# Kernel tuning notes

Measured on AMD Instinct MI355X. Metric: run time of the kernel, lower is better.

## Reference

```python
import jax, jax.numpy as jnp
import numpy as np

N_GENE = 50000
N_PROT = 50000
E = 500000
D = 128          # embedding_dim
C = 32           # out_channels = embedding_dim // attn_heads
F_IN = 256       # in_channels per node type
NUM_MP = 3       # metapaths: [gene-gene, gene-protein, protein-protein]


def _glorot(key, shape):
    lim = float(np.sqrt(6.0 / (shape[0] + shape[1])))
    return jax.random.uniform(key, shape, minval=-lim, maxval=lim, dtype=jnp.float32)


def setup_inputs() -> dict:
    key = jax.random.key(0)
    ks = jax.random.split(key, 24)
    inp = {
        "x_gene": jax.random.normal(ks[0], (N_GENE, F_IN), dtype=jnp.float32),
        "x_protein": jax.random.normal(ks[1], (N_PROT, F_IN), dtype=jnp.float32),
        # node-type projections linear_l / linear_r
        "Wl_gene": _glorot(ks[2], (D, F_IN)), "bl_gene": jnp.zeros((D,), jnp.float32),
        "Wr_gene": _glorot(ks[3], (D, F_IN)), "br_gene": jnp.zeros((D,), jnp.float32),
        "Wl_prot": _glorot(ks[4], (D, F_IN)), "bl_prot": jnp.zeros((D,), jnp.float32),
        "Wr_prot": _glorot(ks[5], (D, F_IN)), "br_prot": jnp.zeros((D,), jnp.float32),
        # per-metapath attention params (stacked over 3 metapaths)
        "alW": jnp.stack([_glorot(ks[6 + i], (C, D)) for i in range(NUM_MP)]),
        "alb": jnp.zeros((NUM_MP, C), jnp.float32),
        "arW": jnp.stack([_glorot(ks[9 + i], (C, D)) for i in range(NUM_MP)]),
        "arb": jnp.zeros((NUM_MP, C), jnp.float32),
        "qw": jnp.stack([_glorot(ks[12 + i], (2 * C, 1)) for i in range(NUM_MP)]),
        "sharp": jnp.ones((NUM_MP,), jnp.float32),  # 'sharpening' alpha_activation
        # per-node-type relation-weighting conv (Linear(D, 1))
        "conv_gene_W": _glorot(ks[15], (1, D)), "conv_gene_b": jnp.zeros((1,), jnp.float32),
        "conv_prot_W": _glorot(ks[16], (1, D)), "conv_prot_b": jnp.zeros((1,), jnp.float32),
        # edge indices: row 0 = head node (aggregation target), row 1 = tail node
        "edge_gg": jax.random.randint(ks[17], (2, E), 0, N_GENE, dtype=jnp.int32),
        "edge_gp": jnp.stack([jax.random.randint(ks[18], (E,), 0, N_GENE, dtype=jnp.int32),
                               jax.random.randint(ks[19], (E,), 0, N_PROT, dtype=jnp.int32)]),
        "edge_pp": jax.random.randint(ks[20], (2, E), 0, N_PROT, dtype=jnp.int32),
    }
    return inp


def _segment_softmax(scores, seg, n):
    # numerically stable softmax over variable-size neighborhoods (grouped by seg)
    m = jax.ops.segment_max(scores, seg, num_segments=n)
    m = jnp.where(jnp.isfinite(m), m, 0.0)
    ex = jnp.exp(scores - m[seg])
    denom = jax.ops.segment_sum(ex, seg, num_segments=n)
    return ex / (denom[seg] + 1e-16)


def _metapath_agg(l_head, r_tail, alW, alb, arW, arb, qw, sharp, eidx, n_head):
    # alpha_l / alpha_r node-level projections [N, C]
    al = l_head @ alW.T + alb
    ar = r_tail @ arW.T + arb
    src, dst = eidx[0], eidx[1]           # head (aggregate-at), tail (message-from)
    a_i = al[src]                          # [E, C]
    a_j = ar[dst]                          # [E, C]
    # attn_q: Tanh then Linear(2C -> 1, no bias); 'sharpening' scales the logit
    e = (jnp.tanh(jnp.concatenate([a_i, a_j], axis=1)) @ qw)[:, 0] * sharp  # [E]
    alpha = _segment_softmax(e, src, n_head)
    # message x_j * alpha, scatter-add into head nodes (aggr='add')
    return jax.ops.segment_sum(r_tail[dst] * alpha[:, None], src, num_segments=n_head)


def _relation_combine(aggs, l_self, conv_W, conv_b):
    # stack relation embeddings + self embedding: [N, R, D]
    out = jnp.stack(aggs + [l_self], axis=1)
    beta = jax.nn.softmax(out @ conv_W.T + conv_b, axis=1)  # [N, R, 1]
    return jax.nn.relu(jnp.sum(out * beta, axis=1))          # [N, D]


def reference(x_gene, x_protein, Wl_gene, bl_gene, Wr_gene, br_gene,
              Wl_prot, bl_prot, Wr_prot, br_prot,
              alW, alb, arW, arb, qw, sharp,
              conv_gene_W, conv_gene_b, conv_prot_W, conv_prot_b,
              edge_gg, edge_gp, edge_pp):
    # first layer: l/r projections from raw features
    l_gene = x_gene @ Wl_gene.T + bl_gene
    r_gene = x_gene @ Wr_gene.T + br_gene
    l_prot = x_protein @ Wl_prot.T + bl_prot
    r_prot = x_protein @ Wr_prot.T + br_prot

    # metapath 0: gene <- gene ; metapath 1: gene <- protein ; metapath 2: protein <- protein
    agg_gg = _metapath_agg(l_gene, r_gene, alW[0], alb[0], arW[0], arb[0], qw[0], sharp[0], edge_gg, N_GENE)
    agg_gp = _metapath_agg(l_gene, r_prot, alW[1], alb[1], arW[1], arb[1], qw[1], sharp[1], edge_gp, N_GENE)
    agg_pp = _metapath_agg(l_prot, r_prot, alW[2], alb[2], arW[2], arb[2], qw[2], sharp[2], edge_pp, N_PROT)

    out_gene = _relation_combine([agg_gg, agg_gp], l_gene, conv_gene_W, conv_gene_b)
    out_prot = _relation_combine([agg_pp], l_prot, conv_prot_W, conv_prot_b)
    return (out_gene, out_prot)
```

## Files before the change

kernel.cpp:

```cpp
#include <hip/hip_runtime.h>
#include <hip/hip_bf16.h>


typedef __attribute__((ext_vector_type(8))) short short8;
typedef __attribute__((ext_vector_type(4))) float floatx4;

__device__ __forceinline__ void gload16(const void* g, void* l) {
  __builtin_amdgcn_global_load_lds(
      (const __attribute__((address_space(1))) void*)g,
      (__attribute__((address_space(3))) void*)l, 16, 0, 0);
}

__device__ __forceinline__ ushort f2b(float x) {
  __hip_bfloat16 h = __float2bfloat16(x);
  return *reinterpret_cast<ushort*>(&h);
}
__device__ __forceinline__ float b2f_lo(unsigned v) { return __uint_as_float(v << 16); }
__device__ __forceinline__ float b2f_hi(unsigned v) { return __uint_as_float(v & 0xffff0000u); }

struct CvtArgs {
  const float* src[8];
  ushort* dst[8];
  int valid[8];
  int total[8];
  int bstart[9];
};
__global__ __launch_bounds__(256) void cvt_multi(CvtArgs a) {
  int b = blockIdx.x;
  int e = 0;
#pragma unroll
  for (int j = 1; j < 8; ++j)
    if (b >= a.bstart[j]) e = j;
  int i = ((b - a.bstart[e]) * 256 + threadIdx.x) * 4;
  if (i >= a.total[e]) return;
  float4 v = make_float4(0.f, 0.f, 0.f, 0.f);
  if (i < a.valid[e]) v = *(const float4*)(a.src[e] + i);
  ushort4 o;
  o.x = f2b(v.x); o.y = f2b(v.y); o.z = f2b(v.z); o.w = f2b(v.w);
  *(ushort4*)(a.dst[e] + i) = o;
}

struct ProjArgs {
  const float* x[2];
  const ushort* Wb[2];
  const float* bl[2];
  const float* br[2];
  ushort* lb[2];
  ushort* rb[2];
  int N[2];
  const ushort* aW[4];
  const float* ab[4];
  const float* q0[4];
  const float* q1[4];
  float* o0[4];
  float* o1[4];
  int BN[4];
  const float* sharp;
  const int* e0;
  const int* e1;
  const int* e2;
  int* deg;
  int* rank;
  int E;
  int NGh;
  int projBlocks;
  int totalBlocks;
};
__global__ __launch_bounds__(256) void proj_lr_mfma(ProjArgs g) {
  __shared__ float Asf[2 * 128 * 32];
  __shared__ ushort Bs[2 * 128 * 32];
  const int tid = threadIdx.x;

  const int P = g.projBlocks, T = g.totalBlocks;
  const int bid = blockIdx.x;
  const int pcntLo = (int)(((long long)bid * P) / T);
  const int pcntHi = (int)(((long long)(bid + 1) * P) / T);
  const bool isProj = pcntHi > pcntLo;

  if (!isProj) {
    const int E = g.E;
    int e = (bid - pcntLo) * 256 + tid;
    if (e < 3 * E) {
      int mp = (e >= 2 * E) ? 2 : ((e >= E) ? 1 : 0);
      int el = e - mp * E;
      const int* ep = (mp == 0) ? g.e0 : (mp == 1) ? g.e1 : g.e2;
      int segb = (mp == 2) ? 2 * g.NGh : mp * g.NGh;
      g.rank[e] = atomicAdd(&g.deg[segb + ep[el]], 1);
    }
    return;
  }

  const int pb = pcntLo;
  const int ty = pb & 1;
  const int colHalf = (pb >> 1) & 1;
  const float* xp = g.x[ty];
  const int N = g.N[ty];
  const int lane = tid & 63;
  const int wv = tid >> 6;
  const int wm = wv & 1, wn = wv >> 1;
  const int rowBase = (pb >> 2) * 128;
  const ushort* Wbase = g.Wb[ty] + (size_t)colHalf * 128 * 256;

  floatx4 acc[4][4] = {};

  auto stage = [&](int buf, int k0) {
#pragma unroll
    for (int i = 0; i < 4; ++i) {
      const int G = i * 256 + wv * 64 + lane;
      const int row = G >> 3;
      const int cg = (G & 7) ^ (row & 7);
      const int xr = min(rowBase + row, N - 1);
      gload16(xp + (size_t)xr * 256 + k0 + cg * 4, &Asf[buf * 4096 + G * 4]);
    }
#pragma unroll
    for (int i = 0; i < 2; ++i) {
      const int G = i * 256 + wv * 64 + lane;
      const int row = G >> 2;
      const int cg = (G & 3) ^ ((row >> 1) & 3);
      gload16(Wbase + (size_t)row * 256 + k0 + cg * 8, &Bs[buf * 4096 + G * 8]);
    }
  };

  stage(0, 0);
  __syncthreads();

  int t = 0;
  for (int k0 = 0; k0 < 256; k0 += 32) {
    if (k0 < 224) stage(t ^ 1, k0 + 32);
    const float* Ab = &Asf[t * 4096];
    const ushort* Bb = &Bs[t * 4096];
    short8 bf[4];
#pragma unroll
    for (int nt = 0; nt < 4; ++nt) {
      const int row = wn * 64 + nt * 16 + (lane & 15);
      const int c = (lane >> 4) ^ ((row >> 1) & 3);
      bf[nt] = *(const short8*)&Bb[(row * 4 + c) * 8];
    }
#pragma unroll
    for (int mt = 0; mt < 4; ++mt) {
      const int row = wm * 64 + mt * 16 + (lane & 15);
      const int c0 = ((lane >> 4) * 2) ^ (row & 7);
      const int c1 = ((lane >> 4) * 2 + 1) ^ (row & 7);
      float4 f0 = *(const float4*)&Ab[(row * 8 + c0) * 4];
      float4 f1 = *(const float4*)&Ab[(row * 8 + c1) * 4];
      short8 a;
      a[0] = (short)f2b(f0.x); a[1] = (short)f2b(f0.y);
      a[2] = (short)f2b(f0.z); a[3] = (short)f2b(f0.w);
      a[4] = (short)f2b(f1.x); a[5] = (short)f2b(f1.y);
      a[6] = (short)f2b(f1.z); a[7] = (short)f2b(f1.w);
#pragma unroll
      for (int nt = 0; nt < 4; ++nt)
        acc[mt][nt] = __builtin_amdgcn_mfma_f32_16x16x32_bf16(a, bf[nt], acc[mt][nt], 0, 0, 0);
    }
    __syncthreads();
    t ^= 1;
  }

  ushort* tile = (ushort*)Asf;
  const float* bias = colHalf ? g.br[ty] : g.bl[ty];
  ushort* outp = colHalf ? g.rb[ty] : g.lb[ty];
#pragma unroll
  for (int mt = 0; mt < 4; ++mt)
#pragma unroll
    for (int nt = 0; nt < 4; ++nt) {
      int col = wn * 64 + nt * 16 + (lane & 15);
      float bv = bias[col];
#pragma unroll
      for (int vi = 0; vi < 4; ++vi) {
        int row = wm * 64 + mt * 16 + (lane >> 4) * 4 + vi;
        ushort v = f2b(acc[mt][nt][vi] + bv);
        if (colHalf)
          tile[row * 128 + (((col >> 3) ^ (row & 15)) << 3) + (col & 7)] = v;
        if (rowBase + row < N) outp[(size_t)(rowBase + row) * 128 + col] = v;
      }
    }
  if (colHalf == 0) return;
  __syncthreads();

  const int e = ty * 2 + colHalf;
  const int NB = g.BN[e] >> 4;
  const ushort* aW = g.aW[e];
  floatx4 acc2[2][4] = {};
  for (int k0 = 0; k0 < 128; k0 += 32) {
    short8 bf2[4];
#pragma unroll
    for (int nt = 0; nt < 4; ++nt)
      if (nt < NB)
        bf2[nt] = *(const short8*)(aW + (size_t)(nt * 16 + (lane & 15)) * 128 +
                                   k0 + (lane >> 4) * 8);
#pragma unroll
    for (int mt = 0; mt < 2; ++mt) {
      const int row = wv * 32 + mt * 16 + (lane & 15);
      const int c8 = (k0 >> 3) + (lane >> 4);
      short8 a = *(const short8*)&tile[row * 128 + ((c8 ^ (row & 15)) << 3)];
#pragma unroll
      for (int nt = 0; nt < 4; ++nt)
        if (nt < NB)
          acc2[mt][nt] = __builtin_amdgcn_mfma_f32_16x16x32_bf16(a, bf2[nt], acc2[mt][nt], 0, 0, 0);
    }
  }

  const float* ab = g.ab[e];
  const int l15 = lane & 15;
  const bool two = (NB == 4);
  const float shLo = (e == 1) ? g.sharp[0] : g.sharp[1];
  const float shHi = g.sharp[2];
  float bv2[4];
#pragma unroll
  for (int nt = 0; nt < 4; ++nt) bv2[nt] = (nt < NB) ? ab[nt * 16 + l15] : 0.f;
  float q0v0 = g.q0[e][l15], q0v1 = g.q0[e][16 + l15];
  float q1v0 = 0.f, q1v1 = 0.f;
  if (two) { q1v0 = g.q1[e][l15]; q1v1 = g.q1[e][16 + l15]; }
  float* o0 = g.o0[e];
  float* o1 = g.o1[e];
#pragma unroll
  for (int mt = 0; mt < 2; ++mt)
#pragma unroll
    for (int vi = 0; vi < 4; ++vi) {
      float slo = tanhf(acc2[mt][0][vi] + bv2[0]) * q0v0
                + tanhf(acc2[mt][1][vi] + bv2[1]) * q0v1;
      float shi = 0.f;
      if (two)
        shi = tanhf(acc2[mt][2][vi] + bv2[2]) * q1v0
            + tanhf(acc2[mt][3][vi] + bv2[3]) * q1v1;
#pragma unroll
      for (int m = 8; m >= 1; m >>= 1) {
        slo += __shfl_xor(slo, m, 64);
        shi += __shfl_xor(shi, m, 64);
      }
      const int row = rowBase + wv * 32 + mt * 16 + (lane >> 4) * 4 + vi;
      if (l15 == 0 && row < N) {
        o0[row] = expf(slo * shLo);
        if (two) o1[row] = expf(shi * shHi);
      }
    }
}

__global__ __launch_bounds__(256) void scanA_kernel(
    const int* __restrict__ deg, int* __restrict__ offsets,
    int* __restrict__ tile_tot, int n) {
  __shared__ int wtot[4];
  const int t = threadIdx.x;
  const int base = blockIdx.x * 2048 + t * 8;
  int v[8], pre[8], s = 0;
#pragma unroll
  for (int j = 0; j < 8; ++j) {
    v[j] = (base + j < n) ? deg[base + j] : 0;
    pre[j] = s;
    s += v[j];
  }
  const int lane = t & 63, wv = t >> 6;
  int x = s;
#pragma unroll
  for (int o = 1; o < 64; o <<= 1) {
    int u = __shfl_up(x, o, 64);
    if (lane >= o) x += u;
  }
  if (lane == 63) wtot[wv] = x;
  __syncthreads();
  int wpre = 0;
#pragma unroll
  for (int j = 0; j < 4; ++j) wpre += (j < wv) ? wtot[j] : 0;
  int excl = wpre + x - s;
#pragma unroll
  for (int j = 0; j < 8; ++j)
    if (base + j < n) offsets[base + j] = excl + pre[j];
  if (t == 255) tile_tot[blockIdx.x] = wpre + x;
}

__global__ __launch_bounds__(256) void scanB_kernel(
    const int* __restrict__ tile_tot, int* __restrict__ tile_pre,
    int* __restrict__ offsets, int T, int n) {
  __shared__ int wtot[4];
  const int t = threadIdx.x;
  int v = (t < T) ? tile_tot[t] : 0;
  const int lane = t & 63, wv = t >> 6;
  int x = v;
#pragma unroll
  for (int o = 1; o < 64; o <<= 1) {
    int u = __shfl_up(x, o, 64);
    if (lane >= o) x += u;
  }
  if (lane == 63) wtot[wv] = x;
  __syncthreads();
  int wpre = 0;
#pragma unroll
  for (int j = 0; j < 4; ++j) wpre += (j < wv) ? wtot[j] : 0;
  if (t < T) tile_pre[t] = wpre + x - v;
  if (t == 255) offsets[n] = wpre + x;
}

__global__ __launch_bounds__(256) void scanC_kernel(
    int* __restrict__ offsets, const int* __restrict__ tile_pre, int n) {
  const int add = tile_pre[blockIdx.x];
  const int base = blockIdx.x * 2048 + threadIdx.x * 8;
#pragma unroll
  for (int j = 0; j < 8; ++j)
    if (base + j < n) offsets[base + j] += add;
}

__global__ __launch_bounds__(256) void scatter3_kernel(
    const int* __restrict__ e0, const int* __restrict__ e1,
    const int* __restrict__ e2, const int* __restrict__ rank,
    const int* __restrict__ offsets,
    const float* __restrict__ etr, int2* __restrict__ recs,
    int E, int NG, int NP) {
  int e = blockIdx.x * 256 + threadIdx.x;
  if (e >= 3 * E) return;
  int mp = (e >= 2 * E) ? 2 : ((e >= E) ? 1 : 0);
  int el = e - mp * E;
  const int* ep = (mp == 0) ? e0 : (mp == 1) ? e1 : e2;
  int s = ep[el], d = ep[el + E];
  int hb = (mp == 2) ? 2 * NG : mp * NG;
  int tb = (mp == 0) ? 0 : (mp == 1) ? NG : NG + NP;
  float w = etr[tb + d];
  recs[offsets[hb + s] + rank[e]] = make_int2(d << 8, __float_as_int(w));
}

__global__ __launch_bounds__(256) void gather_combine(
    const ushort* __restrict__ rb_gene, const ushort* __restrict__ rb_prot,
    const ushort* __restrict__ lb_gene, const ushort* __restrict__ lb_prot,
    const int* __restrict__ offsets, const int2* __restrict__ recs,
    const float* __restrict__ cgW, const float* __restrict__ cgb,
    const float* __restrict__ cpW, const float* __restrict__ cpb,
    float* __restrict__ out_gene, float* __restrict__ out_prot,
    int NG, int NP) {
  const int lane = threadIdx.x & 63;
  const int l16 = lane & 15;
  const int node = blockIdx.x * 16 + (threadIdx.x >> 4);
  if (node >= NG + NP) return;
  const bool isGene = node < NG;
  const unsigned coloff = (unsigned)l16 << 4;
  const unsigned OMASK = 0x00FFFF00u;

  const int h0 = isGene ? node : NG + node;
  const int j0a = offsets[h0];
  const int ca = offsets[h0 + 1] - j0a;
  int j0b = 0, cb2 = 0;
  if (isGene) {
    j0b = offsets[NG + node];
    cb2 = offsets[NG + node + 1] - j0b;
  }

  float a0[8] = {0.f, 0.f, 0.f, 0.f, 0.f, 0.f, 0.f, 0.f};
  float a1[8] = {0.f, 0.f, 0.f, 0.f, 0.f, 0.f, 0.f, 0.f};
  float ds0 = 0.f, ds1 = 0.f;
  const ushort* rtA = isGene ? rb_gene : rb_prot;

  if (isGene) {
    const int cmax = (ca > cb2) ? ca : cb2;
    if (cmax > 0) {
      int2 rA[4], rB[4];
#pragma unroll
      for (int p = 0; p < 4; ++p) {
        rA[p] = recs[j0a + ((p < ca) ? p : 0)];
        rB[p] = recs[j0b + ((p < cb2) ? p : 0)];
      }
      const int nit = (cmax + 3) >> 2;
      for (int it = 0; it < nit; ++it) {
        const int b = it * 4;
        float wA[4], wB[4];
        uint4 vA[4], vB[4];
#pragma unroll
        for (int p = 0; p < 4; ++p) {
          wA[p] = (b + p < ca)  ? __int_as_float(rA[p].y) : 0.f;
          wB[p] = (b + p < cb2) ? __int_as_float(rB[p].y) : 0.f;
          vA[p] = *(const uint4*)((const char*)rtA + (((unsigned)rA[p].x & OMASK) + coloff));
          vB[p] = *(const uint4*)((const char*)rb_prot + (((unsigned)rB[p].x & OMASK) + coloff));
        }
        const int nb = b + 4;
#pragma unroll
        for (int p = 0; p < 4; ++p) {
          rA[p] = recs[j0a + ((nb + p < ca) ? nb + p : 0)];
          rB[p] = recs[j0b + ((nb + p < cb2) ? nb + p : 0)];
        }
#pragma unroll
        for (int p = 0; p < 4; ++p) {
          ds0 += wA[p];
          a0[0] += b2f_lo(vA[p].x) * wA[p]; a0[1] += b2f_hi(vA[p].x) * wA[p];
          a0[2] += b2f_lo(vA[p].y) * wA[p]; a0[3] += b2f_hi(vA[p].y) * wA[p];
          a0[4] += b2f_lo(vA[p].z) * wA[p]; a0[5] += b2f_hi(vA[p].z) * wA[p];
          a0[6] += b2f_lo(vA[p].w) * wA[p]; a0[7] += b2f_hi(vA[p].w) * wA[p];
          ds1 += wB[p];
          a1[0] += b2f_lo(vB[p].x) * wB[p]; a1[1] += b2f_hi(vB[p].x) * wB[p];
          a1[2] += b2f_lo(vB[p].y) * wB[p]; a1[3] += b2f_hi(vB[p].y) * wB[p];
          a1[4] += b2f_lo(vB[p].z) * wB[p]; a1[5] += b2f_hi(vB[p].z) * wB[p];
          a1[6] += b2f_lo(vB[p].w) * wB[p]; a1[7] += b2f_hi(vB[p].w) * wB[p];
        }
      }
    }
  } else {
    if (ca > 0) {
      int2 r0 = recs[j0a];
      int2 r1 = recs[j0a + ((1 < ca) ? 1 : 0)];
      int2 r2 = recs[j0a + ((2 < ca) ? 2 : 0)];
      int2 r3 = recs[j0a + ((3 < ca) ? 3 : 0)];
      const int nit = (ca + 3) >> 2;
      for (int it = 0; it < nit; ++it) {
        const int b = it * 4;
        const float w0 = (b < ca)     ? __int_as_float(r0.y) : 0.f;
        const float w1 = (b + 1 < ca) ? __int_as_float(r1.y) : 0.f;
        const float w2 = (b + 2 < ca) ? __int_as_float(r2.y) : 0.f;
        const float w3 = (b + 3 < ca) ? __int_as_float(r3.y) : 0.f;
        const uint4 v0 = *(const uint4*)((const char*)rtA + (((unsigned)r0.x & OMASK) + coloff));
        const uint4 v1 = *(const uint4*)((const char*)rtA + (((unsigned)r1.x & OMASK) + coloff));
        const uint4 v2 = *(const uint4*)((const char*)rtA + (((unsigned)r2.x & OMASK) + coloff));
        const uint4 v3 = *(const uint4*)((const char*)rtA + (((unsigned)r3.x & OMASK) + coloff));
        const int nb = b + 4;
        r0 = recs[j0a + ((nb < ca) ? nb : 0)];
        r1 = recs[j0a + ((nb + 1 < ca) ? nb + 1 : 0)];
        r2 = recs[j0a + ((nb + 2 < ca) ? nb + 2 : 0)];
        r3 = recs[j0a + ((nb + 3 < ca) ? nb + 3 : 0)];
        ds0 += (w0 + w1) + (w2 + w3);
        a0[0] += b2f_lo(v0.x) * w0 + b2f_lo(v1.x) * w1 + b2f_lo(v2.x) * w2 + b2f_lo(v3.x) * w3;
        a0[1] += b2f_hi(v0.x) * w0 + b2f_hi(v1.x) * w1 + b2f_hi(v2.x) * w2 + b2f_hi(v3.x) * w3;
        a0[2] += b2f_lo(v0.y) * w0 + b2f_lo(v1.y) * w1 + b2f_lo(v2.y) * w2 + b2f_lo(v3.y) * w3;
        a0[3] += b2f_hi(v0.y) * w0 + b2f_hi(v1.y) * w1 + b2f_hi(v2.y) * w2 + b2f_hi(v3.y) * w3;
        a0[4] += b2f_lo(v0.z) * w0 + b2f_lo(v1.z) * w1 + b2f_lo(v2.z) * w2 + b2f_lo(v3.z) * w3;
        a0[5] += b2f_hi(v0.z) * w0 + b2f_hi(v1.z) * w1 + b2f_hi(v2.z) * w2 + b2f_hi(v3.z) * w3;
        a0[6] += b2f_lo(v0.w) * w0 + b2f_lo(v1.w) * w1 + b2f_lo(v2.w) * w2 + b2f_lo(v3.w) * w3;
        a0[7] += b2f_hi(v0.w) * w0 + b2f_hi(v1.w) * w1 + b2f_hi(v2.w) * w2 + b2f_hi(v3.w) * w3;
      }
    }
  }

  const float inv0 = 1.f / (ds0 + 1e-16f);
  const float inv1 = 1.f / (ds1 + 1e-16f);
  float g0[8], g1[8], self[8];
#pragma unroll
  for (int c = 0; c < 8; ++c) { g0[c] = a0[c] * inv0; g1[c] = a1[c] * inv1; }
  {
    const ushort* lbp = isGene ? lb_gene + (size_t)node * 128
                               : lb_prot + (size_t)(node - NG) * 128;
    uint4 sv = *(const uint4*)(lbp + l16 * 8);
    self[0] = b2f_lo(sv.x); self[1] = b2f_hi(sv.x);
    self[2] = b2f_lo(sv.y); self[3] = b2f_hi(sv.y);
    self[4] = b2f_lo(sv.z); self[5] = b2f_hi(sv.z);
    self[6] = b2f_lo(sv.w); self[7] = b2f_hi(sv.w);
  }

  const float* cW = isGene ? cgW : cpW;
  const float cb = isGene ? cgb[0] : cpb[0];
  const float4 wlo = *(const float4*)(cW + l16 * 8);
  const float4 whi = *(const float4*)(cW + l16 * 8 + 4);
  float p0 = g0[0] * wlo.x + g0[1] * wlo.y + g0[2] * wlo.z + g0[3] * wlo.w +
             g0[4] * whi.x + g0[5] * whi.y + g0[6] * whi.z + g0[7] * whi.w;
  float p1 = g1[0] * wlo.x + g1[1] * wlo.y + g1[2] * wlo.z + g1[3] * wlo.w +
             g1[4] * whi.x + g1[5] * whi.y + g1[6] * whi.z + g1[7] * whi.w;
  float ps = self[0] * wlo.x + self[1] * wlo.y + self[2] * wlo.z + self[3] * wlo.w +
             self[4] * whi.x + self[5] * whi.y + self[6] * whi.z + self[7] * whi.w;
#pragma unroll
  for (int m = 8; m >= 1; m >>= 1) {
    p0 += __shfl_xor(p0, m, 64);
    p1 += __shfl_xor(p1, m, 64);
    ps += __shfl_xor(ps, m, 64);
  }
  const float s0 = p0 + cb, s1 = p1 + cb, ss = ps + cb;
  const float mx = isGene ? fmaxf(fmaxf(s0, s1), ss) : fmaxf(s0, ss);
  const float e0 = expf(s0 - mx);
  const float e1 = isGene ? expf(s1 - mx) : 0.f;
  const float es = expf(ss - mx);
  const float sum = e0 + e1 + es;
  const float b0 = e0 / sum, b1 = e1 / sum, bs = es / sum;

  float4 o0, o1;
  o0.x = fmaxf(g0[0] * b0 + g1[0] * b1 + self[0] * bs, 0.f);
  o0.y = fmaxf(g0[1] * b0 + g1[1] * b1 + self[1] * bs, 0.f);
  o0.z = fmaxf(g0[2] * b0 + g1[2] * b1 + self[2] * bs, 0.f);
  o0.w = fmaxf(g0[3] * b0 + g1[3] * b1 + self[3] * bs, 0.f);
  o1.x = fmaxf(g0[4] * b0 + g1[4] * b1 + self[4] * bs, 0.f);
  o1.y = fmaxf(g0[5] * b0 + g1[5] * b1 + self[5] * bs, 0.f);
  o1.z = fmaxf(g0[6] * b0 + g1[6] * b1 + self[6] * bs, 0.f);
  o1.w = fmaxf(g0[7] * b0 + g1[7] * b1 + self[7] * bs, 0.f);
  float* op = isGene ? out_gene + (size_t)node * 128
                     : out_prot + (size_t)(node - NG) * 128;
  *(float4*)(op + l16 * 8) = o0;
  *(float4*)(op + l16 * 8 + 4) = o1;
}

extern "C" void kernel_launch(void* const* d_in, const int* in_sizes, int n_in,
                              void* d_out, int out_size, void* d_ws,
                              size_t ws_size, hipStream_t stream) {
  const float* x_gene  = (const float*)d_in[0];
  const float* x_prot  = (const float*)d_in[1];
  const float* Wl_gene = (const float*)d_in[2];
  const float* bl_gene = (const float*)d_in[3];
  const float* Wr_gene = (const float*)d_in[4];
  const float* br_gene = (const float*)d_in[5];
  const float* Wl_prot = (const float*)d_in[6];
  const float* bl_prot = (const float*)d_in[7];
  const float* Wr_prot = (const float*)d_in[8];
  const float* br_prot = (const float*)d_in[9];
  const float* alW     = (const float*)d_in[10];
  const float* alb     = (const float*)d_in[11];
  const float* arW     = (const float*)d_in[12];
  const float* arb     = (const float*)d_in[13];
  const float* qw      = (const float*)d_in[14];
  const float* sharp   = (const float*)d_in[15];
  const float* cgW     = (const float*)d_in[16];
  const float* cgb     = (const float*)d_in[17];
  const float* cpW     = (const float*)d_in[18];
  const float* cpb     = (const float*)d_in[19];
  const int* e_gg      = (const int*)d_in[20];
  const int* e_gp      = (const int*)d_in[21];
  const int* e_pp      = (const int*)d_in[22];

  const int NG = in_sizes[0] / 256;
  const int NP = in_sizes[1] / 256;
  const int E  = in_sizes[20] / 2;
  const int NPG = (NG + 127) & ~127;
  const int NT = 2 * NG + NP;
  const int NR = NG + 2 * NP;

  char* base = (char*)d_ws;
  size_t off = 0;
  auto alloc = [&](size_t bytes) {
    void* p = base + off;
    off = (off + bytes + 255) & ~(size_t)255;
    return p;
  };
  ushort* Wlr_gene = (ushort*)alloc(256 * 256 * 2);
  ushort* Wlr_prot = (ushort*)alloc(256 * 256 * 2);
  ushort* alWb     = (ushort*)alloc(96 * 128 * 2);
  ushort* arWb     = (ushort*)alloc(96 * 128 * 2);
  ushort* lb_gene  = (ushort*)alloc((size_t)NPG * 128 * 2);
  ushort* rb_gene  = (ushort*)alloc((size_t)NPG * 128 * 2);
  ushort* lb_prot  = (ushort*)alloc((size_t)NPG * 128 * 2);
  ushort* rb_prot  = (ushort*)alloc((size_t)NPG * 128 * 2);
  int*    deg      = (int*)alloc((size_t)NT * 4);
  int*    offsets  = (int*)alloc((size_t)(NT + 1) * 4);
  const int TILES  = (NT + 2047) / 2048;
  int*    tile_tot = (int*)alloc((size_t)TILES * 4);
  int*    tile_pre = (int*)alloc((size_t)TILES * 4);
  int*    rank     = (int*)alloc((size_t)(3 * E) * 4);
  int2*   recs     = (int2*)alloc((size_t)(3 * E) * sizeof(int2));
  float*  etr      = (float*)alloc((size_t)NR * 4);

  float* out_gene = (float*)d_out;
  float* out_prot = out_gene + (size_t)NG * 128;

  dim3 blk(256);

  hipMemsetAsync(deg, 0, (size_t)NT * sizeof(int), stream);
  {
    CvtArgs a;
    const float* srcs[8] = {Wl_gene, Wr_gene, Wl_prot, Wr_prot, alW, arW,
                            Wl_gene, Wl_gene};
    ushort* dsts[8] = {Wlr_gene, Wlr_gene + 128 * 256,
                       Wlr_prot, Wlr_prot + 128 * 256, alWb, arWb,
                       Wlr_gene, Wlr_gene};
    int sizes[8] = {128 * 256, 128 * 256, 128 * 256, 128 * 256,
                    96 * 128, 96 * 128, 0, 0};
    int b = 0;
    for (int j = 0; j < 8; ++j) {
      a.src[j] = srcs[j]; a.dst[j] = dsts[j];
      a.valid[j] = sizes[j]; a.total[j] = sizes[j];
      a.bstart[j] = b;
      b += (sizes[j] / 4 + 255) / 256;
    }
    a.bstart[8] = b;
    cvt_multi<<<b, blk, 0, stream>>>(a);
  }

  const int gridE3 = (3 * E + 255) / 256;
  const int projBlocks = (NPG / 128) * 4;
  {
    ProjArgs p;
    p.x[0] = x_gene; p.x[1] = x_prot;
    p.Wb[0] = Wlr_gene; p.Wb[1] = Wlr_prot;
    p.bl[0] = bl_gene; p.bl[1] = bl_prot;
    p.br[0] = br_gene; p.br[1] = br_prot;
    p.lb[0] = lb_gene; p.lb[1] = lb_prot;
    p.rb[0] = rb_gene; p.rb[1] = rb_prot;
    p.N[0] = NG; p.N[1] = NP;
    p.aW[0] = arWb;            p.ab[0] = arb;      p.BN[0] = 32;
    p.q0[0] = qw + 32; p.q1[0] = qw + 32;  p.o0[0] = etr;          p.o1[0] = etr;
    p.aW[1] = arWb;            p.ab[1] = arb;      p.BN[1] = 32;
    p.q0[1] = qw + 32; p.q1[1] = qw + 32;  p.o0[1] = etr;          p.o1[1] = etr;
    p.aW[2] = arWb + 32 * 128; p.ab[2] = arb + 32; p.BN[2] = 64;
    p.q0[2] = qw + 96; p.q1[2] = qw + 160; p.o0[2] = etr + NG;     p.o1[2] = etr + NG + NP;
    p.aW[3] = arWb + 32 * 128; p.ab[3] = arb + 32; p.BN[3] = 64;
    p.q0[3] = qw + 96; p.q1[3] = qw + 160; p.o0[3] = etr + NG;     p.o1[3] = etr + NG + NP;
    p.sharp = sharp;
    p.e0 = e_gg; p.e1 = e_gp; p.e2 = e_pp;
    p.deg = deg; p.rank = rank; p.E = E; p.NGh = NG;
    p.projBlocks = projBlocks;
    p.totalBlocks = projBlocks + gridE3;
    proj_lr_mfma<<<projBlocks + gridE3, blk, 0, stream>>>(p);
  }

  scanA_kernel<<<TILES, blk, 0, stream>>>(deg, offsets, tile_tot, NT);
  scanB_kernel<<<1, blk, 0, stream>>>(tile_tot, tile_pre, offsets, TILES, NT);
  scanC_kernel<<<TILES, blk, 0, stream>>>(offsets, tile_pre, NT);
  scatter3_kernel<<<gridE3, blk, 0, stream>>>(e_gg, e_gp, e_pp, rank, offsets,
                                              etr, recs, E, NG, NP);

  gather_combine<<<(NG + NP + 15) / 16, blk, 0, stream>>>(
      rb_gene, rb_prot, lb_gene, lb_prot, offsets, recs,
      cgW, cgb, cpW, cpb, out_gene, out_prot, NG, NP);
}
```

Baseline: 362.6 us.

## Fuse CSR scan and scatter into one cooperative kernel; fold deg memset into cvt

Replaces the three scan kernels and the scatter kernel with a single cooperative launch of 1024 blocks that uses grid.sync between phases. The separate memset of the degree array is dropped and the zeroing moves into the existing cvt_multi launch as an extra padded segment with no valid source data. Together these remove several kernel launches and their gaps. In exchange, grid-wide barriers add their own cost, and the scatter phase now runs as a grid-stride loop on fewer blocks.

Result: slower. 728.9 us (+101.0%).

```diff
diff --git a/kernel.cpp b/kernel.cpp
--- a/kernel.cpp
+++ b/kernel.cpp
@@ -1,5 +1,7 @@
 #include <hip/hip_runtime.h>
 #include <hip/hip_bf16.h>
+#include <hip/hip_cooperative_groups.h>
+namespace cg = cooperative_groups;
 
 
 typedef __attribute__((ext_vector_type(8))) short short8;
@@ -236,85 +238,91 @@
     }
 }
 
-__global__ __launch_bounds__(256) void scanA_kernel(
-    const int* __restrict__ deg, int* __restrict__ offsets,
-    int* __restrict__ tile_tot, int n) {
+struct CsrArgs {
+  const int* e0; const int* e1; const int* e2;
+  const int* rank;
+  int* deg;
+  int* offsets;
+  int* tile_tot;
+  int* tile_pre;
+  const float* etr;
+  int2* recs;
+  int E, NG, NP, NT, TILES;
+};
+__global__ __launch_bounds__(256) void csr_fused(CsrArgs a) {
+  cg::grid_group grid = cg::this_grid();
+  const int t = threadIdx.x;
+  const int lane = t & 63, wvv = t >> 6;
   __shared__ int wtot[4];
-  const int t = threadIdx.x;
-  const int base = blockIdx.x * 2048 + t * 8;
-  int v[8], pre[8], s = 0;
-#pragma unroll
-  for (int j = 0; j < 8; ++j) {
-    v[j] = (base + j < n) ? deg[base + j] : 0;
-    pre[j] = s;
-    s += v[j];
-  }
-  const int lane = t & 63, wv = t >> 6;
-  int x = s;
-#pragma unroll
-  for (int o = 1; o < 64; o <<= 1) {
-    int u = __shfl_up(x, o, 64);
-    if (lane >= o) x += u;
-  }
-  if (lane == 63) wtot[wv] = x;
-  __syncthreads();
-  int wpre = 0;
-#pragma unroll
-  for (int j = 0; j < 4; ++j) wpre += (j < wv) ? wtot[j] : 0;
-  int excl = wpre + x - s;
-#pragma unroll
-  for (int j = 0; j < 8; ++j)
-    if (base + j < n) offsets[base + j] = excl + pre[j];
-  if (t == 255) tile_tot[blockIdx.x] = wpre + x;
-}
-
-__global__ __launch_bounds__(256) void scanB_kernel(
-    const int* __restrict__ tile_tot, int* __restrict__ tile_pre,
-    int* __restrict__ offsets, int T, int n) {
-  __shared__ int wtot[4];
-  const int t = threadIdx.x;
-  int v = (t < T) ? tile_tot[t] : 0;
-  const int lane = t & 63, wv = t >> 6;
-  int x = v;
-#pragma unroll
-  for (int o = 1; o < 64; o <<= 1) {
-    int u = __shfl_up(x, o, 64);
-    if (lane >= o) x += u;
-  }
-  if (lane == 63) wtot[wv] = x;
-  __syncthreads();
-  int wpre = 0;
-#pragma unroll
-  for (int j = 0; j < 4; ++j) wpre += (j < wv) ? wtot[j] : 0;
-  if (t < T) tile_pre[t] = wpre + x - v;
-  if (t == 255) offsets[n] = wpre + x;
-}
-
-__global__ __launch_bounds__(256) void scanC_kernel(
-    int* __restrict__ offsets, const int* __restrict__ tile_pre, int n) {
-  const int add = tile_pre[blockIdx.x];
-  const int base = blockIdx.x * 2048 + threadIdx.x * 8;
-#pragma unroll
-  for (int j = 0; j < 8; ++j)
-    if (base + j < n) offsets[base + j] += add;
-}
-
-__global__ __launch_bounds__(256) void scatter3_kernel(
-    const int* __restrict__ e0, const int* __restrict__ e1,
-    const int* __restrict__ e2, const int* __restrict__ rank,
-    const int* __restrict__ offsets,
-    const float* __restrict__ etr, int2* __restrict__ recs,
-    int E, int NG, int NP) {
-  int e = blockIdx.x * 256 + threadIdx.x;
-  if (e >= 3 * E) return;
-  int mp = (e >= 2 * E) ? 2 : ((e >= E) ? 1 : 0);
-  int el = e - mp * E;
-  const int* ep = (mp == 0) ? e0 : (mp == 1) ? e1 : e2;
-  int s = ep[el], d = ep[el + E];
-  int hb = (mp == 2) ? 2 * NG : mp * NG;
-  int tb = (mp == 0) ? 0 : (mp == 1) ? NG : NG + NP;
-  float w = etr[tb + d];
-  recs[offsets[hb + s] + rank[e]] = make_int2(d << 8, __float_as_int(w));
+  const int n = a.NT;
+
+  for (int tile = blockIdx.x; tile < a.TILES; tile += gridDim.x) {
+    const int base = tile * 2048 + t * 8;
+    int v[8], pre[8], s = 0;
+#pragma unroll
+    for (int j = 0; j < 8; ++j) {
+      v[j] = (base + j < n) ? a.deg[base + j] : 0;
+      pre[j] = s;
+      s += v[j];
+    }
+    int x = s;
+#pragma unroll
+    for (int o = 1; o < 64; o <<= 1) {
+      int u = __shfl_up(x, o, 64);
+      if (lane >= o) x += u;
+    }
+    if (lane == 63) wtot[wvv] = x;
+    __syncthreads();
+    int wpre = 0;
+#pragma unroll
+    for (int j = 0; j < 4; ++j) wpre += (j < wvv) ? wtot[j] : 0;
+    int excl = wpre + x - s;
+#pragma unroll
+    for (int j = 0; j < 8; ++j)
+      if (base + j < n) a.offsets[base + j] = excl + pre[j];
+    if (t == 255) a.tile_tot[tile] = wpre + x;
+    __syncthreads();
+  }
+  grid.sync();
+
+  if (blockIdx.x == 0) {
+    int v = (t < a.TILES) ? a.tile_tot[t] : 0;
+    int x = v;
+#pragma unroll
+    for (int o = 1; o < 64; o <<= 1) {
+      int u = __shfl_up(x, o, 64);
+      if (lane >= o) x += u;
+    }
+    if (lane == 63) wtot[wvv] = x;
+    __syncthreads();
+    int wpre = 0;
+#pragma unroll
+    for (int j = 0; j < 4; ++j) wpre += (j < wvv) ? wtot[j] : 0;
+    if (t < a.TILES) a.tile_pre[t] = wpre + x - v;
+    if (t == 255) a.offsets[n] = wpre + x;
+  }
+  grid.sync();
+
+  for (int tile = blockIdx.x; tile < a.TILES; tile += gridDim.x) {
+    const int add = a.tile_pre[tile];
+    const int base = tile * 2048 + t * 8;
+#pragma unroll
+    for (int j = 0; j < 8; ++j)
+      if (base + j < n) a.offsets[base + j] += add;
+  }
+  grid.sync();
+
+  const int E = a.E, NG = a.NG, NP = a.NP;
+  for (int e = blockIdx.x * 256 + t; e < 3 * E; e += gridDim.x * 256) {
+    int mp = (e >= 2 * E) ? 2 : ((e >= E) ? 1 : 0);
+    int el = e - mp * E;
+    const int* ep = (mp == 0) ? a.e0 : (mp == 1) ? a.e1 : a.e2;
+    int s = ep[el], d = ep[el + E];
+    int hb = (mp == 2) ? 2 * NG : mp * NG;
+    int tb = (mp == 0) ? 0 : (mp == 1) ? NG : NG + NP;
+    float w = a.etr[tb + d];
+    a.recs[a.offsets[hb + s] + a.rank[e]] = make_int2(d << 8, __float_as_int(w));
+  }
 }
 
 __global__ __launch_bounds__(256) void gather_combine(
@@ -541,22 +549,23 @@
 
   dim3 blk(256);
 
-  hipMemsetAsync(deg, 0, (size_t)NT * sizeof(int), stream);
   {
     CvtArgs a;
     const float* srcs[8] = {Wl_gene, Wr_gene, Wl_prot, Wr_prot, alW, arW,
                             Wl_gene, Wl_gene};
     ushort* dsts[8] = {Wlr_gene, Wlr_gene + 128 * 256,
                        Wlr_prot, Wlr_prot + 128 * 256, alWb, arWb,
-                       Wlr_gene, Wlr_gene};
-    int sizes[8] = {128 * 256, 128 * 256, 128 * 256, 128 * 256,
-                    96 * 128, 96 * 128, 0, 0};
+                       (ushort*)deg, Wlr_gene};
+    int valids[8] = {128 * 256, 128 * 256, 128 * 256, 128 * 256,
+                     96 * 128, 96 * 128, 0, 0};
+    int totals[8] = {128 * 256, 128 * 256, 128 * 256, 128 * 256,
+                     96 * 128, 96 * 128, NT * 2, 0};
     int b = 0;
     for (int j = 0; j < 8; ++j) {
       a.src[j] = srcs[j]; a.dst[j] = dsts[j];
-      a.valid[j] = sizes[j]; a.total[j] = sizes[j];
+      a.valid[j] = valids[j]; a.total[j] = totals[j];
       a.bstart[j] = b;
-      b += (sizes[j] / 4 + 255) / 256;
+      b += (totals[j] / 4 + 255) / 256;
     }
     a.bstart[8] = b;
     cvt_multi<<<b, blk, 0, stream>>>(a);
@@ -589,11 +598,17 @@
     proj_lr_mfma<<<projBlocks + gridE3, blk, 0, stream>>>(p);
   }
 
-  scanA_kernel<<<TILES, blk, 0, stream>>>(deg, offsets, tile_tot, NT);
-  scanB_kernel<<<1, blk, 0, stream>>>(tile_tot, tile_pre, offsets, TILES, NT);
-  scanC_kernel<<<TILES, blk, 0, stream>>>(offsets, tile_pre, NT);
-  scatter3_kernel<<<gridE3, blk, 0, stream>>>(e_gg, e_gp, e_pp, rank, offsets,
-                                              etr, recs, E, NG, NP);
+  {
+    CsrArgs c;
+    c.e0 = e_gg; c.e1 = e_gp; c.e2 = e_pp;
+    c.rank = rank; c.deg = deg; c.offsets = offsets;
+    c.tile_tot = tile_tot; c.tile_pre = tile_pre;
+    c.etr = etr; c.recs = recs;
+    c.E = E; c.NG = NG; c.NP = NP; c.NT = NT; c.TILES = TILES;
+    void* params[] = {(void*)&c};
+    hipLaunchCooperativeKernel((const void*)csr_fused, dim3(1024), dim3(256),
+                               params, 0, stream);
+  }
 
   gather_combine<<<(NG + NP + 15) / 16, blk, 0, stream>>>(
       rb_gene, rb_prot, lb_gene, lb_prot, offsets, recs,
```
